# Optimization experiments

Measured on AMD Instinct MI355X. Metric: run time of the kernel, lower is better.

## Reference

```python
import jax, jax.numpy as jnp
import numpy as np

WS = 7        # window size (square)
SH = 3        # shift size
NH = 8        # num heads
N = WS * WS   # tokens per window


def _rel_pos_index():
    coords = np.stack(np.meshgrid(np.arange(WS), np.arange(WS), indexing='ij'))
    cf = coords.reshape(2, -1)                      # (2, N)
    rel = cf[:, :, None] - cf[:, None, :]           # (2, N, N)
    rel = rel.transpose(1, 2, 0)
    rel[:, :, 0] += WS - 1
    rel[:, :, 1] += WS - 1
    rel[:, :, 0] *= 2 * WS - 1
    return rel.sum(-1)                              # (N, N) int


def _attn_mask(pH, pW):
    img = np.zeros((pH, pW), dtype=np.float32)
    h_sl = [(0, pH - WS), (pH - WS, pH - SH), (pH - SH, pH)]
    w_sl = [(0, pW - WS), (pW - WS, pW - SH), (pW - SH, pW)]
    cnt = 0
    for h0, h1 in h_sl:
        for w0, w1 in w_sl:
            img[h0:h1, w0:w1] = cnt
            cnt += 1
    m = img.reshape(pH // WS, WS, pW // WS, WS).transpose(0, 2, 1, 3).reshape(-1, N)
    diff = m[:, None, :] - m[:, :, None]            # (nw, N, N)
    return np.where(diff != 0, -100.0, 0.0).astype(np.float32)


def setup_inputs() -> dict:
    key = jax.random.key(0)
    ks = jax.random.split(key, 6)
    C = 256
    return {
        'x': jax.random.normal(ks[0], (32, 56, 56, C), dtype=jnp.float32),
        'qkv_weight': jax.random.normal(ks[1], (3 * C, C), dtype=jnp.float32) * 0.02,
        'qkv_bias': jax.random.normal(ks[2], (3 * C,), dtype=jnp.float32) * 0.02,
        'proj_weight': jax.random.normal(ks[3], (C, C), dtype=jnp.float32) * 0.02,
        'proj_bias': jax.random.normal(ks[4], (C,), dtype=jnp.float32) * 0.02,
        'rpb_table': jax.random.normal(ks[5], ((2 * WS - 1) ** 2, NH), dtype=jnp.float32) * 0.02,
    }


def reference(x, qkv_weight, qkv_bias, proj_weight, proj_bias, rpb_table):
    B, H, W, C = x.shape
    hd = C // NH
    pad_r = (WS - W % WS) % WS
    pad_b = (WS - H % WS) % WS
    xp = jnp.pad(x, ((0, 0), (0, pad_b), (0, pad_r), (0, 0)))
    pH, pW = H + pad_b, W + pad_r
    xp = jnp.roll(xp, shift=(-SH, -SH), axis=(1, 2))
    nw = (pH // WS) * (pW // WS)
    # window partition -> (B*nw, N, C)
    xw = xp.reshape(B, pH // WS, WS, pW // WS, WS, C)
    xw = xw.transpose(0, 1, 3, 2, 4, 5).reshape(B * nw, N, C)
    # qkv projection
    qkv = xw @ qkv_weight.T + qkv_bias                      # (B*nw, N, 3C)
    qkv = qkv.reshape(B * nw, N, 3, NH, hd).transpose(2, 0, 3, 1, 4)
    q, k, v = qkv[0], qkv[1], qkv[2]                        # (B*nw, NH, N, hd)
    q = q * (hd ** -0.5)
    attn = jnp.einsum('bhnd,bhmd->bhnm', q, k)              # (B*nw, NH, N, N)
    # relative position bias
    idx = jnp.asarray(_rel_pos_index())
    bias = rpb_table[idx].transpose(2, 0, 1)                # (NH, N, N)
    attn = attn + bias[None]
    # shift mask
    mask = jnp.asarray(_attn_mask(pH, pW))                  # (nw, N, N)
    attn = attn.reshape(B, nw, NH, N, N) + mask[None, :, None]
    attn = jax.nn.softmax(attn.reshape(B * nw, NH, N, N), axis=-1)
    out = jnp.einsum('bhnm,bhmd->bhnd', attn, v)            # (B*nw, NH, N, hd)
    out = out.transpose(0, 2, 1, 3).reshape(B * nw, N, C)
    out = out @ proj_weight.T + proj_bias
    # window reverse
    out = out.reshape(B, pH // WS, pW // WS, WS, WS, C)
    out = out.transpose(0, 1, 3, 2, 4, 5).reshape(B, pH, pW, C)
    out = jnp.roll(out, shift=(SH, SH), axis=(1, 2))
    return out[:, :H, :W, :]
```

## Files before the change

### kernel.cpp

```cpp
#include <hip/hip_runtime.h>
#include <hip/hip_bf16.h>

typedef __attribute__((ext_vector_type(4))) float f32x4;
typedef __attribute__((ext_vector_type(8))) short s16x8;
typedef __attribute__((ext_vector_type(4))) short s16x4;

#define LXS 264
#define LQS 520
#define LVS 72

#define OFF_LQK   0
#define SZ_LQK    (64 * LQS * 2)
#define OFF_LVT   (OFF_LQK + SZ_LQK)
#define SZ_LVT    (8 * 32 * LVS * 2)
#define OFF_LX    (OFF_LVT + SZ_LVT)
#define SZ_LX     (64 * LXS * 2)
#define OFF_LB    (OFF_LX + SZ_LX)
#define SZ_LB     (169 * 8 * 4)
#define SMEM_BYTES (OFF_LB + SZ_LB)

__device__ __forceinline__ short f2bf(float f) {
    unsigned u = __builtin_bit_cast(unsigned, f);
    unsigned r = (u + 0x7FFFu + ((u >> 16) & 1u)) >> 16;
    return (short)r;
}

__device__ __forceinline__ int region_id(int wy, int wx, int ty, int tx) {
    int rr = wy * 7 + ty;
    int cc = wx * 7 + tx;
    int rh = (rr < 49) ? 0 : ((rr < 53) ? 1 : 2);
    int rw = (cc < 49) ? 0 : ((cc < 53) ? 1 : 2);
    return rh * 3 + rw;
}

__global__ void wcvt_kernel(const float* __restrict__ qw, const float* __restrict__ pw,
                            short* __restrict__ wqkv, short* __restrict__ wproj) {
    int idx = blockIdx.x * blockDim.x + threadIdx.x;
    int stride = gridDim.x * blockDim.x;
    for (int i = idx; i < 65536; i += stride) {
        if (i < 49152) {
            const f32x4 v = *(const f32x4*)(qw + i * 4);
            s16x4 o = { f2bf(v.x), f2bf(v.y), f2bf(v.z), f2bf(v.w) };
            *(s16x4*)(wqkv + i * 4) = o;
        } else {
            int j = i - 49152;
            const f32x4 v = *(const f32x4*)(pw + j * 4);
            s16x4 o = { f2bf(v.x), f2bf(v.y), f2bf(v.z), f2bf(v.w) };
            *(s16x4*)(wproj + j * 4) = o;
        }
    }
}

__global__ __launch_bounds__(512, 2)
void swin_kernel(const float* __restrict__ x,
                 const float* __restrict__ qkv_bias,
                 const float* __restrict__ proj_bias,
                 const float* __restrict__ rpb,
                 const short* __restrict__ wqkv,
                 const short* __restrict__ wproj,
                 float* __restrict__ out) {
    __shared__ __align__(16) char smem[SMEM_BYTES];
    short* lqk   = (short*)(smem + OFF_LQK);
    short* lvT   = (short*)(smem + OFF_LVT);
    short* lx    = (short*)(smem + OFF_LX);
    float* lbias = (float*)(smem + OFF_LB);

    const int tid  = threadIdx.x;
    const int w    = tid >> 6;
    const int lane = tid & 63;
    const int il   = lane & 15;
    const int gl   = lane >> 4;

    const int b   = blockIdx.x >> 6;
    const int wid = blockIdx.x & 63;
    const int wy  = wid >> 3, wx = wid & 7;

    for (int i = tid; i < 1352; i += 512) lbias[i] = rpb[i];
    for (int i = tid; i < 4096; i += 512) {
        int t = i >> 6, c4 = (i & 63) << 2;
        s16x4 o;
        if (t < 49) {
            int ty = t / 7, tx = t % 7;
            int R = wy * 7 + ty + 3; if (R >= 56) R -= 56;
            int C = wx * 7 + tx + 3; if (C >= 56) C -= 56;
            const f32x4 v = *(const f32x4*)(x + (((b * 56 + R) * 56 + C) << 8) + c4);
            o = (s16x4){ f2bf(v.x), f2bf(v.y), f2bf(v.z), f2bf(v.w) };
        } else {
            o = (s16x4){ 0, 0, 0, 0 };
        }
        *(s16x4*)&lx[t * LXS + c4] = o;
    }
    __syncthreads();

    {
        int cb[6];
        cb[0] = 32 * w;       cb[1] = 32 * w + 16;
        cb[2] = 256 + 32 * w; cb[3] = 256 + 32 * w + 16;
        cb[4] = 512 + 32 * w; cb[5] = 512 + 32 * w + 16;
        f32x4 acc[4][6];
        #pragma unroll
        for (int mi = 0; mi < 4; mi++)
            #pragma unroll
            for (int ni = 0; ni < 6; ni++) acc[mi][ni] = (f32x4){0.f, 0.f, 0.f, 0.f};

        for (int k0 = 0; k0 < 256; k0 += 32) {
            s16x8 a[4], bf[6];
            #pragma unroll
            for (int mi = 0; mi < 4; mi++)
                a[mi] = *(const s16x8*)&lx[(mi * 16 + il) * LXS + k0 + 8 * gl];
            #pragma unroll
            for (int ni = 0; ni < 6; ni++)
                bf[ni] = *(const s16x8*)(wqkv + (cb[ni] + il) * 256 + k0 + 8 * gl);
            #pragma unroll
            for (int ni = 0; ni < 6; ni++)
                #pragma unroll
                for (int mi = 0; mi < 4; mi++)
                    acc[mi][ni] = __builtin_amdgcn_mfma_f32_16x16x32_bf16(a[mi], bf[ni], acc[mi][ni], 0, 0, 0);
        }
        #pragma unroll
        for (int ni = 0; ni < 6; ni++) {
            int col = cb[ni] + il;
            float bv = qkv_bias[col];
            if (ni < 4) {
                float scl = (ni < 2) ? 0.17677669529663687f : 1.0f;
                #pragma unroll
                for (int mi = 0; mi < 4; mi++)
                    #pragma unroll
                    for (int r = 0; r < 4; r++)
                        lqk[(mi * 16 + gl * 4 + r) * LQS + col] = f2bf((acc[mi][ni][r] + bv) * scl);
            } else {
                int d = (ni - 4) * 16 + il;
                #pragma unroll
                for (int mi = 0; mi < 4; mi++) {
                    s16x4 pk = { f2bf(acc[mi][ni][0] + bv), f2bf(acc[mi][ni][1] + bv),
                                 f2bf(acc[mi][ni][2] + bv), f2bf(acc[mi][ni][3] + bv) };
                    *(s16x4*)&lvT[(w * 32 + d) * LVS + mi * 16 + gl * 4] = pk;
                }
            }
        }
    }
    __syncthreads();

    const int h = w;
    f32x4 s[4][4];
    {
        s16x8 ak[4], bq[4];
        #pragma unroll
        for (int mi = 0; mi < 4; mi++)
            ak[mi] = *(const s16x8*)&lqk[(mi * 16 + il) * LQS + 256 + 32 * h + 8 * gl];
        #pragma unroll
        for (int ni = 0; ni < 4; ni++)
            bq[ni] = *(const s16x8*)&lqk[(ni * 16 + il) * LQS + 32 * h + 8 * gl];
        #pragma unroll
        for (int mi = 0; mi < 4; mi++)
            #pragma unroll
            for (int ni = 0; ni < 4; ni++)
                s[mi][ni] = __builtin_amdgcn_mfma_f32_16x16x32_bf16(ak[mi], bq[ni], (f32x4){0.f,0.f,0.f,0.f}, 0, 0, 0);
    }
    int yi[4], xi[4], cnti[4];
    #pragma unroll
    for (int ni = 0; ni < 4; ni++) {
        int i = ni * 16 + il; int ic = i > 48 ? 48 : i;
        yi[ni] = ic / 7; xi[ni] = ic % 7;
        cnti[ni] = region_id(wy, wx, yi[ni], xi[ni]);
    }
    float mx[4] = { -1e30f, -1e30f, -1e30f, -1e30f };
    #pragma unroll
    for (int mi = 0; mi < 4; mi++) {
        #pragma unroll
        for (int r = 0; r < 4; r++) {
            int j = mi * 16 + gl * 4 + r;
            bool jok = (j < 49);
            int jc = jok ? j : 48;
            int yj = jc / 7, xj = jc % 7;
            int cj = region_id(wy, wx, yj, xj);
            #pragma unroll
            for (int ni = 0; ni < 4; ni++) {
                float v;
                if (jok) {
                    float bb = lbias[((yi[ni] - yj + 6) * 13 + (xi[ni] - xj + 6)) * 8 + h];
                    v = s[mi][ni][r] + bb + ((cnti[ni] != cj) ? -100.0f : 0.0f);
                } else {
                    v = -1e30f;
                }
                s[mi][ni][r] = v;
                mx[ni] = fmaxf(mx[ni], v);
            }
        }
    }
    #pragma unroll
    for (int ni = 0; ni < 4; ni++) {
        mx[ni] = fmaxf(mx[ni], __shfl_xor(mx[ni], 16));
        mx[ni] = fmaxf(mx[ni], __shfl_xor(mx[ni], 32));
    }
    float sum[4] = { 0.f, 0.f, 0.f, 0.f };
    #pragma unroll
    for (int mi = 0; mi < 4; mi++)
        #pragma unroll
        for (int ni = 0; ni < 4; ni++)
            #pragma unroll
            for (int r = 0; r < 4; r++) {
                float p = __expf(s[mi][ni][r] - mx[ni]);
                s[mi][ni][r] = p;
                sum[ni] += p;
            }
    #pragma unroll
    for (int ni = 0; ni < 4; ni++) {
        sum[ni] += __shfl_xor(sum[ni], 16);
        sum[ni] += __shfl_xor(sum[ni], 32);
        sum[ni] = 1.0f / sum[ni];
    }
    unsigned pkd[4][4][2];
    #pragma unroll
    for (int mi = 0; mi < 4; mi++)
        #pragma unroll
        for (int ni = 0; ni < 4; ni++) {
            float p0 = s[mi][ni][0] * sum[ni], p1 = s[mi][ni][1] * sum[ni];
            float p2 = s[mi][ni][2] * sum[ni], p3 = s[mi][ni][3] * sum[ni];
            pkd[mi][ni][0] = (unsigned)(unsigned short)f2bf(p0) | ((unsigned)(unsigned short)f2bf(p1) << 16);
            pkd[mi][ni][1] = (unsigned)(unsigned short)f2bf(p2) | ((unsigned)(unsigned short)f2bf(p3) << 16);
        }
    f32x4 o[2][4];
    #pragma unroll
    for (int md = 0; md < 2; md++)
        #pragma unroll
        for (int ni = 0; ni < 4; ni++) o[md][ni] = (f32x4){0.f, 0.f, 0.f, 0.f};
    #pragma unroll
    for (int ks = 0; ks < 2; ks++) {
        s16x8 bp[4];
        #pragma unroll
        for (int ni = 0; ni < 4; ni++) {
            unsigned wd[4];
            #pragma unroll
            for (int q = 0; q < 4; q++) {
                int src = (2 * (gl & 1) + (q >> 1)) * 16 + il;
                unsigned v0 = (unsigned)__shfl((int)pkd[2 * ks    ][ni][q & 1], src);
                unsigned v1 = (unsigned)__shfl((int)pkd[2 * ks + 1][ni][q & 1], src);
                wd[q] = (gl & 2) ? v1 : v0;
            }
            union { unsigned u[4]; s16x8 v; } cv;
            cv.u[0] = wd[0]; cv.u[1] = wd[1]; cv.u[2] = wd[2]; cv.u[3] = wd[3];
            bp[ni] = cv.v;
        }
        s16x8 av[2];
        #pragma unroll
        for (int md = 0; md < 2; md++)
            av[md] = *(const s16x8*)&lvT[(h * 32 + md * 16 + il) * LVS + ks * 32 + 8 * gl];
        #pragma unroll
        for (int md = 0; md < 2; md++)
            #pragma unroll
            for (int ni = 0; ni < 4; ni++)
                o[md][ni] = __builtin_amdgcn_mfma_f32_16x16x32_bf16(av[md], bp[ni], o[md][ni], 0, 0, 0);
    }
    #pragma unroll
    for (int md = 0; md < 2; md++)
        #pragma unroll
        for (int ni = 0; ni < 4; ni++) {
            s16x4 pk = { f2bf(o[md][ni][0]), f2bf(o[md][ni][1]), f2bf(o[md][ni][2]), f2bf(o[md][ni][3]) };
            *(s16x4*)&lx[(ni * 16 + il) * LXS + h * 32 + md * 16 + gl * 4] = pk;
        }
    __syncthreads();

    {
        f32x4 acc[4][2];
        #pragma unroll
        for (int mi = 0; mi < 4; mi++)
            #pragma unroll
            for (int ni = 0; ni < 2; ni++) acc[mi][ni] = (f32x4){0.f, 0.f, 0.f, 0.f};
        for (int k0 = 0; k0 < 256; k0 += 32) {
            s16x8 a[4], bw[2];
            #pragma unroll
            for (int mi = 0; mi < 4; mi++)
                a[mi] = *(const s16x8*)&lx[(mi * 16 + il) * LXS + k0 + 8 * gl];
            #pragma unroll
            for (int ni = 0; ni < 2; ni++)
                bw[ni] = *(const s16x8*)(wproj + (32 * w + 16 * ni + il) * 256 + k0 + 8 * gl);
            #pragma unroll
            for (int mi = 0; mi < 4; mi++)
                #pragma unroll
                for (int ni = 0; ni < 2; ni++)
                    acc[mi][ni] = __builtin_amdgcn_mfma_f32_16x16x32_bf16(a[mi], bw[ni], acc[mi][ni], 0, 0, 0);
        }
        #pragma unroll
        for (int ni = 0; ni < 2; ni++) {
            int oc = 32 * w + 16 * ni + il;
            float pb = proj_bias[oc];
            #pragma unroll
            for (int mi = 0; mi < 4; mi++)
                #pragma unroll
                for (int r = 0; r < 4; r++) {
                    int t = mi * 16 + gl * 4 + r;
                    if (t < 49) {
                        int ty = t / 7, tx = t % 7;
                        int R = wy * 7 + ty + 3; if (R >= 56) R -= 56;
                        int C = wx * 7 + tx + 3; if (C >= 56) C -= 56;
                        out[(((b * 56 + R) * 56 + C) << 8) + oc] = acc[mi][ni][r] + pb;
                    }
                }
        }
    }
}

extern "C" void kernel_launch(void* const* d_in, const int* in_sizes, int n_in,
                              void* d_out, int out_size, void* d_ws, size_t ws_size,
                              hipStream_t stream) {
    const float* x   = (const float*)d_in[0];
    const float* qw  = (const float*)d_in[1];
    const float* qb  = (const float*)d_in[2];
    const float* pw  = (const float*)d_in[3];
    const float* pb  = (const float*)d_in[4];
    const float* rpb = (const float*)d_in[5];

    short* wqkv  = (short*)d_ws;
    short* wproj = wqkv + 768 * 256;

    wcvt_kernel<<<128, 256, 0, stream>>>(qw, pw, wqkv, wproj);
    swin_kernel<<<2048, 512, 0, stream>>>(x, qb, pb, rpb, wqkv, wproj, (float*)d_out);
}
```

Measured before the change: 257.9 us.

## Alias shared buffers and keep V in registers to fit four blocks per CU

Merges the separate x, QK and V^T shared-memory regions into one aliased buffer, adding extra barriers so phases do not overwrite live data. V is no longer stored transposed in LDS. It stays packed in registers and is redistributed with cross-lane shuffles, the same way P is. Launch bounds go from 2 to 4 blocks per CU to raise occupancy, which squeezes the register budget and may cause spills. Weight-fragment loads are also interleaved with the MFMAs to shorten register live ranges.

```diff
diff --git a/kernel.cpp b/kernel.cpp
--- a/kernel.cpp
+++ b/kernel.cpp
@@ -5,24 +5,21 @@
 typedef __attribute__((ext_vector_type(8))) short s16x8;
 typedef __attribute__((ext_vector_type(4))) short s16x4;
 
-#define LXS 264
 #define LQS 520
-#define LVS 72
-
-#define OFF_LQK   0
-#define SZ_LQK    (64 * LQS * 2)
-#define OFF_LVT   (OFF_LQK + SZ_LQK)
-#define SZ_LVT    (8 * 32 * LVS * 2)
-#define OFF_LX    (OFF_LVT + SZ_LVT)
-#define SZ_LX     (64 * LXS * 2)
-#define OFF_LB    (OFF_LX + SZ_LX)
+
+#define SZ_BUF    (64 * LQS * 2)
+#define OFF_LB    SZ_BUF
 #define SZ_LB     (169 * 8 * 4)
-#define SMEM_BYTES (OFF_LB + SZ_LB)
+#define SMEM_BYTES (SZ_BUF + SZ_LB)
 
 __device__ __forceinline__ short f2bf(float f) {
     unsigned u = __builtin_bit_cast(unsigned, f);
     unsigned r = (u + 0x7FFFu + ((u >> 16) & 1u)) >> 16;
     return (short)r;
+}
+
+__device__ __forceinline__ unsigned pk2bf(float a, float b) {
+    return (unsigned)(unsigned short)f2bf(a) | ((unsigned)(unsigned short)f2bf(b) << 16);
 }
 
 __device__ __forceinline__ int region_id(int wy, int wx, int ty, int tx) {
@@ -51,7 +48,7 @@
     }
 }
 
-__global__ __launch_bounds__(512, 2)
+__global__ __launch_bounds__(512, 4)
 void swin_kernel(const float* __restrict__ x,
                  const float* __restrict__ qkv_bias,
                  const float* __restrict__ proj_bias,
@@ -60,9 +57,7 @@
                  const short* __restrict__ wproj,
                  float* __restrict__ out) {
     __shared__ __align__(16) char smem[SMEM_BYTES];
-    short* lqk   = (short*)(smem + OFF_LQK);
-    short* lvT   = (short*)(smem + OFF_LVT);
-    short* lx    = (short*)(smem + OFF_LX);
+    short* buf   = (short*)smem;
     float* lbias = (float*)(smem + OFF_LB);
 
     const int tid  = threadIdx.x;
@@ -88,10 +83,11 @@
         } else {
             o = (s16x4){ 0, 0, 0, 0 };
         }
-        *(s16x4*)&lx[t * LXS + c4] = o;
+        *(s16x4*)&buf[t * LQS + c4] = o;
     }
     __syncthreads();
 
+    unsigned pv[4][2][2];
     {
         int cb[6];
         cb[0] = 32 * w;       cb[1] = 32 * w + 16;
@@ -104,38 +100,38 @@
             for (int ni = 0; ni < 6; ni++) acc[mi][ni] = (f32x4){0.f, 0.f, 0.f, 0.f};
 
         for (int k0 = 0; k0 < 256; k0 += 32) {
-            s16x8 a[4], bf[6];
+            s16x8 a[4];
             #pragma unroll
             for (int mi = 0; mi < 4; mi++)
-                a[mi] = *(const s16x8*)&lx[(mi * 16 + il) * LXS + k0 + 8 * gl];
-            #pragma unroll
-            for (int ni = 0; ni < 6; ni++)
-                bf[ni] = *(const s16x8*)(wqkv + (cb[ni] + il) * 256 + k0 + 8 * gl);
-            #pragma unroll
-            for (int ni = 0; ni < 6; ni++)
+                a[mi] = *(const s16x8*)&buf[(mi * 16 + il) * LQS + k0 + 8 * gl];
+            #pragma unroll
+            for (int ni = 0; ni < 6; ni++) {
+                s16x8 bfr = *(const s16x8*)(wqkv + (cb[ni] + il) * 256 + k0 + 8 * gl);
                 #pragma unroll
                 for (int mi = 0; mi < 4; mi++)
-                    acc[mi][ni] = __builtin_amdgcn_mfma_f32_16x16x32_bf16(a[mi], bf[ni], acc[mi][ni], 0, 0, 0);
-        }
-        #pragma unroll
-        for (int ni = 0; ni < 6; ni++) {
+                    acc[mi][ni] = __builtin_amdgcn_mfma_f32_16x16x32_bf16(a[mi], bfr, acc[mi][ni], 0, 0, 0);
+            }
+        }
+        __syncthreads();
+
+        #pragma unroll
+        for (int ni = 0; ni < 4; ni++) {
             int col = cb[ni] + il;
             float bv = qkv_bias[col];
-            if (ni < 4) {
-                float scl = (ni < 2) ? 0.17677669529663687f : 1.0f;
+            float scl = (ni < 2) ? 0.17677669529663687f : 1.0f;
+            #pragma unroll
+            for (int mi = 0; mi < 4; mi++)
                 #pragma unroll
-                for (int mi = 0; mi < 4; mi++)
-                    #pragma unroll
-                    for (int r = 0; r < 4; r++)
-                        lqk[(mi * 16 + gl * 4 + r) * LQS + col] = f2bf((acc[mi][ni][r] + bv) * scl);
-            } else {
-                int d = (ni - 4) * 16 + il;
-                #pragma unroll
-                for (int mi = 0; mi < 4; mi++) {
-                    s16x4 pk = { f2bf(acc[mi][ni][0] + bv), f2bf(acc[mi][ni][1] + bv),
-                                 f2bf(acc[mi][ni][2] + bv), f2bf(acc[mi][ni][3] + bv) };
-                    *(s16x4*)&lvT[(w * 32 + d) * LVS + mi * 16 + gl * 4] = pk;
-                }
+                for (int r = 0; r < 4; r++)
+                    buf[(mi * 16 + gl * 4 + r) * LQS + col] = f2bf((acc[mi][ni][r] + bv) * scl);
+        }
+        #pragma unroll
+        for (int md = 0; md < 2; md++) {
+            float bv = qkv_bias[cb[4 + md] + il];
+            #pragma unroll
+            for (int mi = 0; mi < 4; mi++) {
+                pv[mi][md][0] = pk2bf(acc[mi][4 + md][0] + bv, acc[mi][4 + md][1] + bv);
+                pv[mi][md][1] = pk2bf(acc[mi][4 + md][2] + bv, acc[mi][4 + md][3] + bv);
             }
         }
     }
@@ -147,10 +143,11 @@
         s16x8 ak[4], bq[4];
         #pragma unroll
         for (int mi = 0; mi < 4; mi++)
-            ak[mi] = *(const s16x8*)&lqk[(mi * 16 + il) * LQS + 256 + 32 * h + 8 * gl];
+            ak[mi] = *(const s16x8*)&buf[(mi * 16 + il) * LQS + 256 + 32 * h + 8 * gl];
         #pragma unroll
         for (int ni = 0; ni < 4; ni++)
-            bq[ni] = *(const s16x8*)&lqk[(ni * 16 + il) * LQS + 32 * h + 8 * gl];
+            bq[ni] = *(const s16x8*)&buf[(ni * 16 + il) * LQS + 32 * h + 8 * gl];
+        __syncthreads();
         #pragma unroll
         for (int mi = 0; mi < 4; mi++)
             #pragma unroll
@@ -215,10 +212,8 @@
     for (int mi = 0; mi < 4; mi++)
         #pragma unroll
         for (int ni = 0; ni < 4; ni++) {
-            float p0 = s[mi][ni][0] * sum[ni], p1 = s[mi][ni][1] * sum[ni];
-            float p2 = s[mi][ni][2] * sum[ni], p3 = s[mi][ni][3] * sum[ni];
-            pkd[mi][ni][0] = (unsigned)(unsigned short)f2bf(p0) | ((unsigned)(unsigned short)f2bf(p1) << 16);
-            pkd[mi][ni][1] = (unsigned)(unsigned short)f2bf(p2) | ((unsigned)(unsigned short)f2bf(p3) << 16);
+            pkd[mi][ni][0] = pk2bf(s[mi][ni][0] * sum[ni], s[mi][ni][1] * sum[ni]);
+            pkd[mi][ni][1] = pk2bf(s[mi][ni][2] * sum[ni], s[mi][ni][3] * sum[ni]);
         }
     f32x4 o[2][4];
     #pragma unroll
@@ -227,7 +222,7 @@
         for (int ni = 0; ni < 4; ni++) o[md][ni] = (f32x4){0.f, 0.f, 0.f, 0.f};
     #pragma unroll
     for (int ks = 0; ks < 2; ks++) {
-        s16x8 bp[4];
+        s16x8 bp[4], av[2];
         #pragma unroll
         for (int ni = 0; ni < 4; ni++) {
             unsigned wd[4];
@@ -242,10 +237,20 @@
             cv.u[0] = wd[0]; cv.u[1] = wd[1]; cv.u[2] = wd[2]; cv.u[3] = wd[3];
             bp[ni] = cv.v;
         }
-        s16x8 av[2];
-        #pragma unroll
-        for (int md = 0; md < 2; md++)
-            av[md] = *(const s16x8*)&lvT[(h * 32 + md * 16 + il) * LVS + ks * 32 + 8 * gl];
+        #pragma unroll
+        for (int md = 0; md < 2; md++) {
+            unsigned wd[4];
+            #pragma unroll
+            for (int q = 0; q < 4; q++) {
+                int src = (2 * (gl & 1) + (q >> 1)) * 16 + il;
+                unsigned v0 = (unsigned)__shfl((int)pv[2 * ks    ][md][q & 1], src);
+                unsigned v1 = (unsigned)__shfl((int)pv[2 * ks + 1][md][q & 1], src);
+                wd[q] = (gl & 2) ? v1 : v0;
+            }
+            union { unsigned u[4]; s16x8 v; } cv;
+            cv.u[0] = wd[0]; cv.u[1] = wd[1]; cv.u[2] = wd[2]; cv.u[3] = wd[3];
+            av[md] = cv.v;
+        }
         #pragma unroll
         for (int md = 0; md < 2; md++)
             #pragma unroll
@@ -257,7 +262,7 @@
         #pragma unroll
         for (int ni = 0; ni < 4; ni++) {
             s16x4 pk = { f2bf(o[md][ni][0]), f2bf(o[md][ni][1]), f2bf(o[md][ni][2]), f2bf(o[md][ni][3]) };
-            *(s16x4*)&lx[(ni * 16 + il) * LXS + h * 32 + md * 16 + gl * 4] = pk;
+            *(s16x4*)&buf[(ni * 16 + il) * LQS + h * 32 + md * 16 + gl * 4] = pk;
         }
     __syncthreads();
 
@@ -268,18 +273,17 @@
             #pragma unroll
             for (int ni = 0; ni < 2; ni++) acc[mi][ni] = (f32x4){0.f, 0.f, 0.f, 0.f};
         for (int k0 = 0; k0 < 256; k0 += 32) {
-            s16x8 a[4], bw[2];
+            s16x8 a[4];
             #pragma unroll
             for (int mi = 0; mi < 4; mi++)
-                a[mi] = *(const s16x8*)&lx[(mi * 16 + il) * LXS + k0 + 8 * gl];
-            #pragma unroll
-            for (int ni = 0; ni < 2; ni++)
-                bw[ni] = *(const s16x8*)(wproj + (32 * w + 16 * ni + il) * 256 + k0 + 8 * gl);
-            #pragma unroll
-            for (int mi = 0; mi < 4; mi++)
+                a[mi] = *(const s16x8*)&buf[(mi * 16 + il) * LQS + k0 + 8 * gl];
+            #pragma unroll
+            for (int ni = 0; ni < 2; ni++) {
+                s16x8 bw = *(const s16x8*)(wproj + (32 * w + 16 * ni + il) * 256 + k0 + 8 * gl);
                 #pragma unroll
-                for (int ni = 0; ni < 2; ni++)
-                    acc[mi][ni] = __builtin_amdgcn_mfma_f32_16x16x32_bf16(a[mi], bw[ni], acc[mi][ni], 0, 0, 0);
+                for (int mi = 0; mi < 4; mi++)
+                    acc[mi][ni] = __builtin_amdgcn_mfma_f32_16x16x32_bf16(a[mi], bw, acc[mi][ni], 0, 0, 0);
+            }
         }
         #pragma unroll
         for (int ni = 0; ni < 2; ni++) {
```

Result: slower. 603.6 us (+134.0%).
